# Kernel optimization log

Hardware: AMD Instinct MI355X
Metric: run time of the kernel (lower is better)

## Reference

```python
import jax, jax.numpy as jnp
import numpy as np
from jax import lax
from jax.scipy.special import logsumexp

ALPHA = 0.8   # weight on shape (soft-DTW) term; (1-ALPHA) on temporal term
GAMMA = 0.01  # soft-DTW smoothing
G = 0.05      # exponential time-weighting rate
BIG = 1e8     # finite stand-in for +inf (keeps gradients NaN-free)


def _softdtw(D, gamma):
    """Soft-DTW value R[N,N] for a single [N,N] cost matrix.
    DP over the 2N-1 anti-diagonals, each diagonal vectorized over rows.
    """
    N = D.shape[0]
    idx = jnp.arange(1, N + 1)  # row indices i of interior cells
    # diagonals k-2 and k-1, stored as length-(N+1) vectors indexed by i
    r2 = jnp.full(N + 1, BIG, D.dtype).at[0].set(0.0)  # holds R[0,0]=0
    r1 = jnp.full(N + 1, BIG, D.dtype)

    def step(carry, k):
        r2, r1 = carry
        j = k + 2 - idx                      # column index for each row on diag k
        valid = (j >= 1) & (j <= N)
        d = jnp.where(valid, D[idx - 1, jnp.clip(j - 1, 0, N - 1)], 0.0)
        a = r2[idx - 1]   # R[i-1, j-1]
        b = r1[idx - 1]   # R[i-1, j]
        c = r1[idx]       # R[i,   j-1]
        sm = -gamma * logsumexp(jnp.stack([-a, -b, -c]) / gamma, axis=0)
        new = jnp.concatenate([jnp.full((1,), BIG, D.dtype),
                               jnp.where(valid, d + sm, BIG)])
        return (r1, new), None

    (_, last), _ = lax.scan(step, (r2, r1), jnp.arange(2 * N - 1))
    return last[N]  # R[N, N]


def _weighted_cost(input, target):
    """Exp-time-weighted pairwise squared-Euclidean cost, [B, N, N]."""
    N = input.shape[1]
    # D[b,i,j] = ||target[b,i] - input[b,j]||^2
    D = jnp.sum((target[:, :, None, :] - input[:, None, :, :]) ** 2, axis=-1)
    w = jnp.exp(G * jnp.arange(N, dtype=D.dtype))
    w = w * (N / jnp.sum(w))  # normalize to mean 1
    return D * w[None, :, None]


def setup_inputs() -> dict:
    key = jax.random.key(0)
    k1, k2 = jax.random.split(key)
    inp = jax.random.normal(k1, (64, 512, 1), dtype=jnp.float32)
    tgt = jax.random.normal(k2, (64, 512, 1), dtype=jnp.float32)
    return {"input": inp, "target": tgt}


def reference(input, target):
    B, N, _ = input.shape
    Dw = _weighted_cost(input, target)  # [B, N, N]
    # shape term: mean soft-DTW value
    loss_shape = jnp.mean(jax.vmap(lambda d: _softdtw(d, GAMMA))(Dw))
    # temporal term: soft alignment path E = dR/dD, penalized by time distortion
    path = jax.vmap(jax.grad(lambda d: _softdtw(d, GAMMA)))(Dw)  # [B, N, N]
    t = jnp.arange(1, N + 1, dtype=Dw.dtype)
    Omega = (t[:, None] - t[None, :]) ** 2  # squared time offsets
    loss_temporal = jnp.mean(jnp.sum(path * Omega, axis=(1, 2))) / (N * N)
    return ALPHA * loss_shape + (1.0 - ALPHA) * loss_temporal
```

## Files before the change

kernel.cpp:

```cpp
#include <hip/hip_runtime.h>
#include <cstddef>
#include <cstdint>

namespace {

constexpr int   kN = 512;
constexpr int   kB = 64;
constexpr float kAlpha = 0.8f;
constexpr float kKexp = 144.26950408889634f;
constexpr float kGLn2 = 0.006931471805599453f;
constexpr float kWexp = 0.07213475204444817f;
constexpr float kZBig = -1.4426950408889634e10f;

constexpr int W     = 8;
constexpr int DELTA = 8;
constexpr int LAM   = 72;
constexpr int SMAX  = 574;
constexpr int NSUP  = 135;
constexpr int BUFE  = 592;

__device__ __forceinline__ float dpp_oldshr1(float oldv, float src) {
    const int oi = __builtin_bit_cast(int, oldv);
    const int si = __builtin_bit_cast(int, src);
    const int r  = __builtin_amdgcn_update_dpp(oi, si, 0x138, 0xF, 0xF, false);
    return __builtin_bit_cast(float, r);
}

__global__ __launch_bounds__(512, 2)
void dilate_jvp8(const float* __restrict__ input,
                 const float* __restrict__ target,
                 float* __restrict__ partials,
                 int b0)
{
    __shared__ float  sx[kN + 16];
    __shared__ float2 buf[W + 1][BUFE];
    __shared__ float  sred[W];

    const int tid = (int)threadIdx.x;
    const int w = tid >> 6, u = tid & 63;
    const bool topw = (w == 0);
    const int b = b0 + (int)blockIdx.x;
    const int sOff = w * LAM;

    sx[tid] = input[(size_t)b * kN + tid];
    if (tid < 16) sx[kN + tid] = 0.0f;
    for (int i = tid; i < BUFE; i += 512) buf[0][i] = make_float2(kZBig, 0.0f);
    const float tk = target[(size_t)b * kN + tid];

    float ew = exp2f(kWexp * (float)tid);
    float es = ew;
    #pragma unroll
    for (int off = 32; off; off >>= 1) es += __shfl_xor(es, off);
    if (u == 0) sred[w] = es;
    __syncthreads();
    float tot = 0.0f;
    #pragma unroll
    for (int q = 0; q < W; ++q) tot += sred[q];
    const float wkz = ew * (512.0f / tot) * (-kKexp);

    float C0 = kZBig, C0d = 0.0f;
    float bval = kZBig, bvald = 0.0f;
    float aval = (topw && u == 0) ? 0.0f : kZBig;
    float avald = 0.0f;
    float xj = sx[0], xjn = sx[(u == 0) ? 1 : 0];
    float fdr = (float)(64 * w + 2 * u);
    const float2* __restrict__ bufP = buf[w];
    float2* __restrict__ bufN = buf[w + 1];

    for (int m = 0; m < NSUP; ++m) {
        const int base = m * DELTA - sOff;
        if (base >= 64 && base <= 504) {
            #pragma unroll
            for (int dg = 0; dg < DELTA; ++dg) {
                const int s = base + dg;
                const float zm = fmaxf(bval, fmaxf(aval, C0));
                const float eA = exp2f(aval - zm);
                const float eB = exp2f(bval - zm);
                const float eC = exp2f(C0   - zm);
                const float ss = eA + eB + eC;
                const float ri = __builtin_amdgcn_rcpf(ss);
                const float dx = tk - xj;
                const float zcur = fmaf(wkz * dx, dx, zm + __log2f(ss));
                const float sd = fmaf(eA, avald, fmaf(eB, bvald, eC * C0d));
                const float curd = fmaf(ri, sd, fdr * fdr);
                C0 = zcur; C0d = curd;
                bufN[s - u] = make_float2(zcur, curd);
                aval = bval; avald = bvald;
                const float2 rn = bufP[s + 1];
                bval  = dpp_oldshr1(rn.x, zcur);
                bvald = dpp_oldshr1(rn.y, curd);
                xj = xjn;
                xjn = sx[s + 2 - u];
                fdr -= 1.0f;
            }
        } else if (base >= -DELTA && base <= SMAX) {
            #pragma unroll
            for (int dg = 0; dg < DELTA; ++dg) {
                const int s = base + dg;
                if (s == -1) {
                    const float2 r0 = bufP[0];
                    bval  = dpp_oldshr1(r0.x, kZBig);
                    bvald = dpp_oldshr1(r0.y, 0.0f);
                } else if (s >= 0 && s <= SMAX) {
                    const int c = s - u;
                    const bool valid = (c >= 0) & (c <= 511);
                    const float zm = fmaxf(bval, fmaxf(aval, C0));
                    const float eA = exp2f(aval - zm);
                    const float eB = exp2f(bval - zm);
                    const float eC = exp2f(C0   - zm);
                    const float ss = eA + eB + eC;
                    const float ri = __builtin_amdgcn_rcpf(ss);
                    const float dx = tk - xj;
                    float zcur = fmaf(wkz * dx, dx, zm + __log2f(ss));
                    const float sd = fmaf(eA, avald, fmaf(eB, bvald, eC * C0d));
                    float curd = fmaf(ri, sd, fdr * fdr);
                    zcur = valid ? zcur : kZBig;
                    curd = valid ? curd : 0.0f;
                    C0 = zcur; C0d = curd;
                    if (c >= 0) bufN[c] = make_float2(zcur, curd);
                    aval = bval; avald = bvald;
                    const float2 rn = bufP[s + 1];
                    bval  = dpp_oldshr1(rn.x, zcur);
                    bvald = dpp_oldshr1(rn.y, curd);
                    xj = xjn;
                    int cc = s + 2 - u;
                    cc = cc < 0 ? 0 : (cc > 511 ? 511 : cc);
                    xjn = sx[cc];
                    fdr -= 1.0f;
                }
            }
        }
        __syncthreads();
    }

    if (tid == 511) {
        const float rnn = C0 * (-kGLn2);
        const float temporal = C0d * (1.0f / (512.0f * 512.0f));
        partials[b] = (kAlpha * rnn + (1.0f - kAlpha) * temporal)
                    * (1.0f / (float)kB);
    }
}

__global__ void dilate_finalize(const float* __restrict__ partials,
                                float* __restrict__ out) {
    float v = partials[threadIdx.x];
    #pragma unroll
    for (int off = 32; off > 0; off >>= 1) v += __shfl_down(v, off);
    if (threadIdx.x == 0) out[0] = v;
}

}

extern "C" void kernel_launch(void* const* d_in, const int* in_sizes, int n_in,
                              void* d_out, int out_size, void* d_ws, size_t ws_size,
                              hipStream_t stream) {
    (void)in_sizes; (void)n_in; (void)out_size; (void)ws_size;
    const float* input  = (const float*)d_in[0];
    const float* target = (const float*)d_in[1];
    float* out      = (float*)d_out;
    float* partials = (float*)d_ws;

    hipLaunchKernelGGL(dilate_jvp8, dim3(kB), dim3(512), 0, stream,
                       input, target, partials, 0);
    hipLaunchKernelGGL(dilate_finalize, dim3(1), dim3(64), 0, stream,
                       partials, out);
}
```

Measured before the change: 202.2 us.

## Process two adjacent columns per thread step in the soft-DTW wavefront

Measured after the change: 241.6 us. +19.4%, slower.

```diff
diff --git a/kernel.cpp b/kernel.cpp
--- a/kernel.cpp
+++ b/kernel.cpp
@@ -15,9 +15,9 @@
 constexpr int W     = 8;
 constexpr int DELTA = 8;
 constexpr int LAM   = 72;
-constexpr int SMAX  = 574;
-constexpr int NSUP  = 135;
-constexpr int BUFE  = 592;
+constexpr int SMAX  = 318;
+constexpr int NSUP  = 103;
+constexpr int BUFP  = 336;
 
 __device__ __forceinline__ float dpp_oldshr1(float oldv, float src) {
     const int oi = __builtin_bit_cast(int, oldv);
@@ -27,13 +27,13 @@
 }
 
 __global__ __launch_bounds__(512, 2)
-void dilate_jvp8(const float* __restrict__ input,
-                 const float* __restrict__ target,
-                 float* __restrict__ partials,
-                 int b0)
+void dilate_jvp_pair(const float* __restrict__ input,
+                     const float* __restrict__ target,
+                     float* __restrict__ partials,
+                     int b0)
 {
     __shared__ float  sx[kN + 16];
-    __shared__ float2 buf[W + 1][BUFE];
+    __shared__ float4 buf[W + 1][BUFP];
     __shared__ float  sred[W];
 
     const int tid = (int)threadIdx.x;
@@ -44,7 +44,8 @@
 
     sx[tid] = input[(size_t)b * kN + tid];
     if (tid < 16) sx[kN + tid] = 0.0f;
-    for (int i = tid; i < BUFE; i += 512) buf[0][i] = make_float2(kZBig, 0.0f);
+    for (int i = tid; i < BUFP; i += 512)
+        buf[0][i] = make_float4(kZBig, 0.0f, kZBig, 0.0f);
     const float tk = target[(size_t)b * kN + tid];
 
     float ew = exp2f(kWexp * (float)tid);
@@ -59,79 +60,86 @@
     const float wkz = ew * (512.0f / tot) * (-kKexp);
 
     float C0 = kZBig, C0d = 0.0f;
-    float bval = kZBig, bvald = 0.0f;
-    float aval = (topw && u == 0) ? 0.0f : kZBig;
-    float avald = 0.0f;
-    float xj = sx[0], xjn = sx[(u == 0) ? 1 : 0];
-    float fdr = (float)(64 * w + 2 * u);
-    const float2* __restrict__ bufP = buf[w];
-    float2* __restrict__ bufN = buf[w + 1];
+    float B0 = kZBig, B0d = 0.0f;
+    float B1 = kZBig, B1d = 0.0f;
+    float pA = (topw && u == 0) ? 0.0f : kZBig;
+    float pAd = 0.0f;
+    const float2* __restrict__ sxp = reinterpret_cast<const float2*>(sx);
+    float2 xp = sxp[0], xpn = sxp[(u == 0) ? 1 : 0];
+    float fdr = (float)(64 * w + 3 * u);
+    const float4* __restrict__ bufP4 = buf[w];
+    float4* __restrict__ bufN4 = buf[w + 1];
+
+#define PAIR_CELLS(VALID_CHECKED)                                           \
+    const float zm0 = fmaxf(B0, fmaxf(pA, C0));                             \
+    const float eA0 = exp2f(pA - zm0);                                      \
+    const float eB0 = exp2f(B0 - zm0);                                      \
+    const float eC0 = exp2f(C0 - zm0);                                      \
+    const float ss0 = eA0 + eB0 + eC0;                                      \
+    const float ri0 = __builtin_amdgcn_rcpf(ss0);                           \
+    const float dx0 = tk - xp.x;                                            \
+    float z0 = fmaf(wkz * dx0, dx0, zm0 + __log2f(ss0));                    \
+    const float sd0 = fmaf(eA0, pAd, fmaf(eB0, B0d, eC0 * C0d));            \
+    float d0 = fmaf(ri0, sd0, fdr * fdr);                                   \
+    if (VALID_CHECKED) { z0 = valid ? z0 : kZBig; d0 = valid ? d0 : 0.0f; } \
+    const float zm1 = fmaxf(B1, fmaxf(B0, z0));                             \
+    const float eA1 = exp2f(B0 - zm1);                                      \
+    const float eB1 = exp2f(B1 - zm1);                                      \
+    const float eC1 = exp2f(z0 - zm1);                                      \
+    const float ss1 = eA1 + eB1 + eC1;                                      \
+    const float ri1 = __builtin_amdgcn_rcpf(ss1);                           \
+    const float dx1 = tk - xp.y;                                            \
+    float z1 = fmaf(wkz * dx1, dx1, zm1 + __log2f(ss1));                    \
+    const float fd1 = fdr - 1.0f;                                           \
+    const float sd1 = fmaf(eA1, B0d, fmaf(eB1, B1d, eC1 * d0));             \
+    float d1 = fmaf(ri1, sd1, fd1 * fd1);                                   \
+    if (VALID_CHECKED) { z1 = valid ? z1 : kZBig; d1 = valid ? d1 : 0.0f; } \
+    C0 = z1; C0d = d1;                                                      \
+    pA = B1; pAd = B1d;
 
     for (int m = 0; m < NSUP; ++m) {
         const int base = m * DELTA - sOff;
-        if (base >= 64 && base <= 504) {
+        if (base >= 64 && base <= 248) {
             #pragma unroll
             for (int dg = 0; dg < DELTA; ++dg) {
-                const int s = base + dg;
-                const float zm = fmaxf(bval, fmaxf(aval, C0));
-                const float eA = exp2f(aval - zm);
-                const float eB = exp2f(bval - zm);
-                const float eC = exp2f(C0   - zm);
-                const float ss = eA + eB + eC;
-                const float ri = __builtin_amdgcn_rcpf(ss);
-                const float dx = tk - xj;
-                const float zcur = fmaf(wkz * dx, dx, zm + __log2f(ss));
-                const float sd = fmaf(eA, avald, fmaf(eB, bvald, eC * C0d));
-                const float curd = fmaf(ri, sd, fdr * fdr);
-                C0 = zcur; C0d = curd;
-                bufN[s - u] = make_float2(zcur, curd);
-                aval = bval; avald = bvald;
-                const float2 rn = bufP[s + 1];
-                bval  = dpp_oldshr1(rn.x, zcur);
-                bvald = dpp_oldshr1(rn.y, curd);
-                xj = xjn;
-                xjn = sx[s + 2 - u];
-                fdr -= 1.0f;
+                const int t = base + dg;
+                const bool valid = true; (void)valid;
+                PAIR_CELLS(false)
+                bufN4[t - u] = make_float4(z0, d0, z1, d1);
+                const float4 rn = bufP4[t + 1];
+                B0 = dpp_oldshr1(rn.x, z0); B0d = dpp_oldshr1(rn.y, d0);
+                B1 = dpp_oldshr1(rn.z, z1); B1d = dpp_oldshr1(rn.w, d1);
+                xp = xpn;
+                xpn = sxp[t + 2 - u];
+                fdr -= 2.0f;
             }
         } else if (base >= -DELTA && base <= SMAX) {
             #pragma unroll
             for (int dg = 0; dg < DELTA; ++dg) {
-                const int s = base + dg;
-                if (s == -1) {
-                    const float2 r0 = bufP[0];
-                    bval  = dpp_oldshr1(r0.x, kZBig);
-                    bvald = dpp_oldshr1(r0.y, 0.0f);
-                } else if (s >= 0 && s <= SMAX) {
-                    const int c = s - u;
-                    const bool valid = (c >= 0) & (c <= 511);
-                    const float zm = fmaxf(bval, fmaxf(aval, C0));
-                    const float eA = exp2f(aval - zm);
-                    const float eB = exp2f(bval - zm);
-                    const float eC = exp2f(C0   - zm);
-                    const float ss = eA + eB + eC;
-                    const float ri = __builtin_amdgcn_rcpf(ss);
-                    const float dx = tk - xj;
-                    float zcur = fmaf(wkz * dx, dx, zm + __log2f(ss));
-                    const float sd = fmaf(eA, avald, fmaf(eB, bvald, eC * C0d));
-                    float curd = fmaf(ri, sd, fdr * fdr);
-                    zcur = valid ? zcur : kZBig;
-                    curd = valid ? curd : 0.0f;
-                    C0 = zcur; C0d = curd;
-                    if (c >= 0) bufN[c] = make_float2(zcur, curd);
-                    aval = bval; avald = bvald;
-                    const float2 rn = bufP[s + 1];
-                    bval  = dpp_oldshr1(rn.x, zcur);
-                    bvald = dpp_oldshr1(rn.y, curd);
-                    xj = xjn;
-                    int cc = s + 2 - u;
-                    cc = cc < 0 ? 0 : (cc > 511 ? 511 : cc);
-                    xjn = sx[cc];
-                    fdr -= 1.0f;
+                const int t = base + dg;
+                if (t == -1) {
+                    const float4 r0 = bufP4[0];
+                    B0 = dpp_oldshr1(r0.x, kZBig); B0d = dpp_oldshr1(r0.y, 0.0f);
+                    B1 = dpp_oldshr1(r0.z, kZBig); B1d = dpp_oldshr1(r0.w, 0.0f);
+                } else if (t >= 0 && t <= SMAX) {
+                    const int p = t - u;
+                    const bool valid = (p >= 0) & (p <= 255);
+                    PAIR_CELLS(true)
+                    if (p >= 0) bufN4[p] = make_float4(z0, d0, z1, d1);
+                    const float4 rn = bufP4[t + 1];
+                    B0 = dpp_oldshr1(rn.x, z0); B0d = dpp_oldshr1(rn.y, d0);
+                    B1 = dpp_oldshr1(rn.z, z1); B1d = dpp_oldshr1(rn.w, d1);
+                    xp = xpn;
+                    int cc = t + 2 - u;
+                    cc = cc < 0 ? 0 : (cc > 257 ? 257 : cc);
+                    xpn = sxp[cc];
+                    fdr -= 2.0f;
                 }
             }
         }
         __syncthreads();
     }
+#undef PAIR_CELLS
 
     if (tid == 511) {
         const float rnn = C0 * (-kGLn2);
@@ -160,7 +168,7 @@
     float* out      = (float*)d_out;
     float* partials = (float*)d_ws;
 
-    hipLaunchKernelGGL(dilate_jvp8, dim3(kB), dim3(512), 0, stream,
+    hipLaunchKernelGGL(dilate_jvp_pair, dim3(kB), dim3(512), 0, stream,
                        input, target, partials, 0);
     hipLaunchKernelGGL(dilate_finalize, dim3(1), dim3(64), 0, stream,
                        partials, out);
```
